# Performance work log

Measured on AMD Instinct MI355X. Metric: run time of the kernel, lower is better.

The kernel has to match this reference:

```python
import jax, jax.numpy as jnp
import numpy as np

BATCH = 2048
K = 64          # num_clusters
D = 128         # latent_dim / cluster_dim
R1 = 1024
OUT_LEN = 512   # output_length
IN_LEN = 512    # input_length
MIN_CLAMP = 0.0


def setup_inputs() -> dict:
    key = jax.random.key(0)
    k1, k2, k3, k4, k5, k6 = jax.random.split(key, 6)
    z = jax.random.normal(k1, (BATCH, 1, D), dtype=jnp.float32)
    u = jax.random.normal(k2, (BATCH, 1, R1), dtype=jnp.float32)
    member = jax.random.uniform(k3, (BATCH, 1, K), dtype=jnp.float32)
    # parameters
    mu = jax.random.uniform(k4, (K, D), dtype=jnp.float32)  # 1 * torch.rand
    sigma_inv = 10.0 * jnp.broadcast_to(jnp.eye(D, dtype=jnp.float32), (K, D, D))  # zeros with diag 10
    # nn.Linear default init: U(-1/sqrt(fan_in), 1/sqrt(fan_in)), weight shape (out, in)
    bound = 1.0 / np.sqrt(R1)
    W_con = jax.random.uniform(k5, (K, OUT_LEN, R1), dtype=jnp.float32, minval=-bound, maxval=bound)
    W_recon = jax.random.uniform(k6, (K, IN_LEN, R1), dtype=jnp.float32, minval=-bound, maxval=bound)
    return {"z": z, "u": u, "member": member, "mu": mu, "sigma_inv": sigma_inv,
            "W_con": W_con, "W_recon": W_recon}


def _compute_psi(z, mu, sigma_inv):
    # z: (B,1,D), mu: (K,D) -> d: (B,K,D)
    d = mu[None, :, :] - z
    # S = sigma_inv @ sigma_inv^T per cluster: (K,D,D)
    S = jnp.einsum('kde,kfe->kdf', sigma_inv, sigma_inv)
    # Mahalanobis: d^T S d per (b,k)
    d2 = jnp.einsum('bkd,kde,bke->bk', d, S, d)
    d2 = jnp.maximum(d2, MIN_CLAMP)
    psi = jax.nn.softmax(-d2, axis=1)  # (B,K)
    return psi


def reference(z, u, member, mu, sigma_inv, W_con, W_recon):
    psi = _compute_psi(z, mu, sigma_inv)          # (B,K)
    u2 = u[:, 0, :]                                # (B,R1)
    # grouped GEMM + abs: per-cluster |Linear(u)|
    y_LLM = jnp.abs(jnp.einsum('bi,koi->bko', u2, W_con))    # (B,K,OUT_LEN)
    x_LLM = jnp.abs(jnp.einsum('bi,koi->bko', u2, W_recon))  # (B,K,IN_LEN)
    mem = member[:, 0, :]                          # (B,K)
    y_con = jnp.einsum('bk,bko->bo', psi, y_LLM)[:, None, :]   # (B,1,OUT_LEN)
    x_recon = jnp.einsum('bk,bko->bo', mem, x_LLM)[:, None, :]  # (B,1,IN_LEN)
    return (y_con, x_recon)
```

## Files before the change

### kernel.cpp

```cpp
#include <hip/hip_runtime.h>
#include <hip/hip_bf16.h>
#include <stdint.h>

typedef __bf16 bf16_t;
typedef __bf16 bf16x8 __attribute__((ext_vector_type(8)));
typedef __bf16 bf16x4 __attribute__((ext_vector_type(4)));
typedef float  v4f    __attribute__((ext_vector_type(4)));
typedef float  f32x4  __attribute__((ext_vector_type(4)));

#define GLDS16(gp, lp)                                                         \
  __builtin_amdgcn_global_load_lds(                                            \
      (__attribute__((address_space(1))) void*)(gp),                           \
      (__attribute__((address_space(3))) void*)(lp), 16, 0, 0)

#define BATCH 2048
#define KEXP  64
#define NOUT  512
#define R1    1024

__global__ __launch_bounds__(256) void cast_u_k(const float* __restrict__ u,
                                                bf16_t* __restrict__ ub) {
  int idx = blockIdx.x * 256 + threadIdx.x;
  float4 v = ((const float4*)u)[idx];
  bf16x4 o;
  o.x = (bf16_t)v.x; o.y = (bf16_t)v.y; o.z = (bf16_t)v.z; o.w = (bf16_t)v.w;
  ((bf16x4*)ub)[idx] = o;
}

__global__ __launch_bounds__(256) void cast_w_k(const float* __restrict__ wcon,
                                                const float* __restrict__ wrec,
                                                bf16_t* __restrict__ wb) {
  const size_t tid = (size_t)blockIdx.x * 256 + threadIdx.x;
#pragma unroll
  for (int it = 0; it < 8; ++it) {
    size_t idx = tid + (size_t)it * (8192u * 256u);
    size_t e = idx << 2;
    int k = (int)(e >> 20);
    int n = (int)((e >> 10) & 1023);
    int i = (int)(e & 1023);
    const float* src = (n < NOUT)
        ? (wcon + (((size_t)k * NOUT + n) << 10) + i)
        : (wrec + (((size_t)k * NOUT + (n - NOUT)) << 10) + i);
    f32x4 v = __builtin_nontemporal_load((const f32x4*)src);
    bf16x4 o;
    o.x = (bf16_t)v.x; o.y = (bf16_t)v.y; o.z = (bf16_t)v.z; o.w = (bf16_t)v.w;
    ((bf16x4*)wb)[idx] = o;
  }
}

__global__ __launch_bounds__(256) void psi_d2_k(const float* __restrict__ z,
                                                const float* __restrict__ mu,
                                                const float* __restrict__ sig,
                                                float* __restrict__ d2g) {
  __shared__ float dv[64][132];
  __shared__ float Ss[16][128];
  const int t = threadIdx.x;
  const int k = blockIdx.x;
  const int b0 = blockIdx.y * 64;

  const float* muk = mu + k * 128;
#pragma unroll
  for (int i = 0; i < 8; ++i) {
    int f4 = i * 256 + t;
    int row = f4 >> 5, c4 = f4 & 31;
    float4 zq = ((const float4*)(z + (size_t)(b0 + row) * 128))[c4];
    float4 mq = ((const float4*)muk)[c4];
    float4 dq;
    dq.x = mq.x - zq.x; dq.y = mq.y - zq.y;
    dq.z = mq.z - zq.z; dq.w = mq.w - zq.w;
    *(float4*)&dv[row][c4 * 4] = dq;
  }

  const int et = t & 15, bt = t >> 4;
  const float* Sk = sig + ((size_t)k << 14);
  float acc[4][8];
#pragma unroll
  for (int j = 0; j < 4; ++j)
#pragma unroll
    for (int i = 0; i < 8; ++i) acc[j][i] = 0.f;

  for (int dblk = 0; dblk < 8; ++dblk) {
    __syncthreads();
#pragma unroll
    for (int i = 0; i < 2; ++i) {
      int f4 = i * 256 + t;
      int row = f4 >> 5, c4 = f4 & 31;
      *(float4*)&Ss[row][c4 * 4] =
          ((const float4*)(Sk + (size_t)(dblk * 16 + row) * 128))[c4];
    }
    __syncthreads();

#pragma unroll
    for (int d4 = 0; d4 < 4; ++d4) {
      float4 a[4];
#pragma unroll
      for (int j = 0; j < 4; ++j)
        a[j] = *(const float4*)&dv[bt * 4 + j][dblk * 16 + d4 * 4];
#pragma unroll
      for (int dd = 0; dd < 4; ++dd) {
        float4 s0 = *(const float4*)&Ss[d4 * 4 + dd][et * 8];
        float4 s1 = *(const float4*)&Ss[d4 * 4 + dd][et * 8 + 4];
        float av[4] = {a[0][dd], a[1][dd], a[2][dd], a[3][dd]};
#pragma unroll
        for (int j = 0; j < 4; ++j) {
          acc[j][0] = fmaf(s0.x, av[j], acc[j][0]);
          acc[j][1] = fmaf(s0.y, av[j], acc[j][1]);
          acc[j][2] = fmaf(s0.z, av[j], acc[j][2]);
          acc[j][3] = fmaf(s0.w, av[j], acc[j][3]);
          acc[j][4] = fmaf(s1.x, av[j], acc[j][4]);
          acc[j][5] = fmaf(s1.y, av[j], acc[j][5]);
          acc[j][6] = fmaf(s1.z, av[j], acc[j][6]);
          acc[j][7] = fmaf(s1.w, av[j], acc[j][7]);
        }
      }
    }
  }

  float v2[4];
#pragma unroll
  for (int j = 0; j < 4; ++j) {
    float s = 0.f;
#pragma unroll
    for (int i = 0; i < 8; ++i) s = fmaf(acc[j][i], acc[j][i], s);
    v2[j] = s;
  }
#pragma unroll
  for (int j = 0; j < 4; ++j) {
    v2[j] += __shfl_xor(v2[j], 1);
    v2[j] += __shfl_xor(v2[j], 2);
    v2[j] += __shfl_xor(v2[j], 4);
    v2[j] += __shfl_xor(v2[j], 8);
  }
  if (et == 0) {
#pragma unroll
    for (int j = 0; j < 4; ++j)
      d2g[(size_t)(b0 + bt * 4 + j) * 64 + k] = v2[j];
  }
}

__global__ __launch_bounds__(256) void psi_sm_k(const float* __restrict__ d2g,
                                                float* __restrict__ psi) {
  const int b = blockIdx.x * 4 + (threadIdx.x >> 6);
  const int lane = threadIdx.x & 63;
  float x = fmaxf(d2g[(size_t)b * 64 + lane], 0.0f);
  float m = x;
  m = fminf(m, __shfl_xor(m, 1));  m = fminf(m, __shfl_xor(m, 2));
  m = fminf(m, __shfl_xor(m, 4));  m = fminf(m, __shfl_xor(m, 8));
  m = fminf(m, __shfl_xor(m, 16)); m = fminf(m, __shfl_xor(m, 32));
  float ex = __expf(m - x);
  float s = ex;
  s += __shfl_xor(s, 1);  s += __shfl_xor(s, 2);  s += __shfl_xor(s, 4);
  s += __shfl_xor(s, 8);  s += __shfl_xor(s, 16); s += __shfl_xor(s, 32);
  psi[(size_t)b * 64 + lane] = ex / s;
}

__global__ __launch_bounds__(256, 2)
void fused_gemm(const bf16_t* __restrict__ ub,
                const bf16_t* __restrict__ wb,
                const float* __restrict__ psi,
                const float* __restrict__ member,
                float* __restrict__ out) {
  __shared__ bf16_t Alds[128 * 64];
  __shared__ bf16_t Blds[128 * 64];
  __shared__ float wlds[128];

  const int t = threadIdx.x, lane = t & 63, wv = t >> 6;
  const int bm0 = blockIdx.x * 128;
  const int n0  = blockIdx.y * 128;
  const int e0  = blockIdx.z * 8;
  const bool is_y = (n0 < NOUT);
  const float* wsel = is_y ? psi : member;
  const int wm = wv & 1, wn = wv >> 1;
  const int l15 = lane & 15, quad = lane >> 4;

  v4f acc[4][4], oacc[4][4];
#pragma unroll
  for (int mi = 0; mi < 4; ++mi)
#pragma unroll
    for (int ni = 0; ni < 4; ++ni)
#pragma unroll
      for (int r = 0; r < 4; ++r) { acc[mi][ni][r] = 0.f; oacc[mi][ni][r] = 0.f; }

  const int rA = wv * 8 + (lane >> 3);
  const int c8 = (((lane & 7) ^ (lane >> 3)) * 8);
  const bf16_t* au  = ub + (size_t)(bm0 + rA) * R1 + c8;
  const bf16_t* bw0 = wb + (size_t)(n0 + rA) * R1 + c8;

  const int fsw = l15 & 7;

  for (int ke = 0; ke < 8; ++ke) {
    const int ex = e0 + ke;
    const bf16_t* bw = bw0 + ((size_t)ex << 20);
    for (int kk = 0; kk < R1; kk += 64) {
      __syncthreads();
      if (kk == 0 && t < 128) wlds[t] = wsel[(size_t)(bm0 + t) * 64 + ex];
#pragma unroll
      for (int j = 0; j < 4; ++j) {
        GLDS16(au + (size_t)(j * 32) * R1 + kk, &Alds[(j * 32 + wv * 8) * 64]);
        GLDS16(bw + (size_t)(j * 32) * R1 + kk, &Blds[(j * 32 + wv * 8) * 64]);
      }
      __syncthreads();

      const bf16_t* Ab = &Alds[(wm * 64 + l15) * 64];
      const bf16_t* Bb = &Blds[(wn * 64 + l15) * 64];
#pragma unroll
      for (int ks = 0; ks < 2; ++ks) {
        const int co = ((ks * 4 + quad) ^ fsw) * 8;
        bf16x8 af[4], bfr[4];
#pragma unroll
        for (int i = 0; i < 4; ++i) {
          af[i]  = *(const bf16x8*)(Ab + i * 16 * 64 + co);
          bfr[i] = *(const bf16x8*)(Bb + i * 16 * 64 + co);
        }
#pragma unroll
        for (int mi = 0; mi < 4; ++mi)
#pragma unroll
          for (int ni = 0; ni < 4; ++ni)
            acc[mi][ni] = __builtin_amdgcn_mfma_f32_16x16x32_bf16(
                af[mi], bfr[ni], acc[mi][ni], 0, 0, 0);
      }
    }
#pragma unroll
    for (int mi = 0; mi < 4; ++mi) {
      float wr[4];
#pragma unroll
      for (int r = 0; r < 4; ++r) wr[r] = wlds[wm * 64 + mi * 16 + quad * 4 + r];
#pragma unroll
      for (int ni = 0; ni < 4; ++ni)
#pragma unroll
        for (int r = 0; r < 4; ++r) {
          oacc[mi][ni][r] += fabsf(acc[mi][ni][r]) * wr[r];
          acc[mi][ni][r] = 0.f;
        }
    }
  }

  float* obase = is_y ? out : out + (size_t)BATCH * NOUT;
  const int oc = (is_y ? n0 : n0 - NOUT) + wn * 64 + l15;
#pragma unroll
  for (int mi = 0; mi < 4; ++mi)
#pragma unroll
    for (int ni = 0; ni < 4; ++ni)
#pragma unroll
      for (int r = 0; r < 4; ++r) {
        int brow = bm0 + wm * 64 + mi * 16 + quad * 4 + r;
        atomicAdd(&obase[(size_t)brow * NOUT + oc + ni * 16], oacc[mi][ni][r]);
      }
}

extern "C" void kernel_launch(void* const* d_in, const int* in_sizes, int n_in,
                              void* d_out, int out_size, void* d_ws, size_t ws_size,
                              hipStream_t stream) {
  const float* z    = (const float*)d_in[0];
  const float* u    = (const float*)d_in[1];
  const float* mem  = (const float*)d_in[2];
  const float* mu   = (const float*)d_in[3];
  const float* sig  = (const float*)d_in[4];
  const float* wcon = (const float*)d_in[5];
  const float* wrec = (const float*)d_in[6];
  float* out = (float*)d_out;

  char* ws = (char*)d_ws;
  bf16_t* ub  = (bf16_t*)ws;
  bf16_t* wb  = (bf16_t*)(ws + ((size_t)4 << 20));
  float*  psw = (float*)(ws + ((size_t)132 << 20));
  float*  d2g = (float*)(ws + ((size_t)132 << 20) + ((size_t)512 << 10));

  hipMemsetAsync(d_out, 0, (size_t)out_size * sizeof(float), stream);
  cast_u_k<<<2048, 256, 0, stream>>>(u, ub);
  cast_w_k<<<8192, 256, 0, stream>>>(wcon, wrec, wb);
  psi_d2_k<<<dim3(64, 32), 256, 0, stream>>>(z, mu, sig, d2g);
  psi_sm_k<<<512, 256, 0, stream>>>(d2g, psw);
  fused_gemm<<<dim3(16, 8, 8), 256, 0, stream>>>(ub, wb, psw, mem, out);
}
```

Measured before the change: 677.8 us.

## Double-buffer LDS tiles with async prefetch and halve the expert-split grid

Moves the fused grouped GEMM from a single LDS buffer with two barriers per k-step to a two-stage software pipeline. Global-to-LDS loads for step s+2 are issued between the two MFMA halves, and explicit waitcnt, sched_barrier and setprio control the ordering. Each block now handles 16 experts instead of 8, which halves the grid and the number of output atomics, and all per-expert weights are loaded into LDS once at the start. This doubles LDS use and leaves fewer blocks, which may lower occupancy or CU coverage, and the hand-written waitcnt accounting is easy to get wrong.

```diff
diff --git a/kernel.cpp b/kernel.cpp
--- a/kernel.cpp
+++ b/kernel.cpp
@@ -160,18 +160,19 @@
                 const float* __restrict__ psi,
                 const float* __restrict__ member,
                 float* __restrict__ out) {
-  __shared__ bf16_t Alds[128 * 64];
-  __shared__ bf16_t Blds[128 * 64];
-  __shared__ float wlds[128];
+  __shared__ bf16_t Alds[2][128 * 64];
+  __shared__ bf16_t Blds[2][128 * 64];
+  __shared__ float  wlds[16][128];
 
   const int t = threadIdx.x, lane = t & 63, wv = t >> 6;
   const int bm0 = blockIdx.x * 128;
   const int n0  = blockIdx.y * 128;
-  const int e0  = blockIdx.z * 8;
+  const int e0  = blockIdx.z * 16;
   const bool is_y = (n0 < NOUT);
   const float* wsel = is_y ? psi : member;
   const int wm = wv & 1, wn = wv >> 1;
   const int l15 = lane & 15, quad = lane >> 4;
+  const int fsw = l15 & 7;
 
   v4f acc[4][4], oacc[4][4];
 #pragma unroll
@@ -186,45 +187,96 @@
   const bf16_t* au  = ub + (size_t)(bm0 + rA) * R1 + c8;
   const bf16_t* bw0 = wb + (size_t)(n0 + rA) * R1 + c8;
 
-  const int fsw = l15 & 7;
-
-  for (int ke = 0; ke < 8; ++ke) {
-    const int ex = e0 + ke;
-    const bf16_t* bw = bw0 + ((size_t)ex << 20);
-    for (int kk = 0; kk < R1; kk += 64) {
-      __syncthreads();
-      if (kk == 0 && t < 128) wlds[t] = wsel[(size_t)(bm0 + t) * 64 + ex];
-#pragma unroll
-      for (int j = 0; j < 4; ++j) {
-        GLDS16(au + (size_t)(j * 32) * R1 + kk, &Alds[(j * 32 + wv * 8) * 64]);
-        GLDS16(bw + (size_t)(j * 32) * R1 + kk, &Blds[(j * 32 + wv * 8) * 64]);
+  const int aoff = (wm * 64 + l15) * 64;
+  const int boff = (wn * 64 + l15) * 64;
+  const int co0 = (quad ^ fsw) * 8;
+  const int co1 = ((4 + quad) ^ fsw) * 8;
+
+  auto STAGE = [&](int s2, int p) {
+    const int ex2 = e0 + (s2 >> 4);
+    const int kk2 = (s2 & 15) << 6;
+    const bf16_t* a = au + kk2;
+    const bf16_t* b = bw0 + ((size_t)ex2 << 20) + kk2;
+    bf16_t* Ad = &Alds[p][wv * 8 * 64];
+    bf16_t* Bd = &Blds[p][wv * 8 * 64];
+#pragma unroll
+    for (int j = 0; j < 4; ++j)
+      GLDS16(a + (size_t)(j * 32) * R1, Ad + j * 32 * 64);
+#pragma unroll
+    for (int j = 0; j < 4; ++j)
+      GLDS16(b + (size_t)(j * 32) * R1, Bd + j * 32 * 64);
+  };
+
+  {
+    const int r = t >> 1, h = (t & 1) * 8;
+    const float* src = wsel + (size_t)(bm0 + r) * 64 + e0 + h;
+    f32x4 v0 = *(const f32x4*)src;
+    f32x4 v1 = *(const f32x4*)(src + 4);
+#pragma unroll
+    for (int j = 0; j < 4; ++j) { wlds[h + j][r] = v0[j]; wlds[h + 4 + j][r] = v1[j]; }
+  }
+  STAGE(0, 0);
+  STAGE(1, 1);
+  asm volatile("s_waitcnt vmcnt(8) lgkmcnt(0)" ::: "memory");
+  __builtin_amdgcn_s_barrier();
+
+  for (int ke = 0; ke < 16; ++ke) {
+#pragma unroll 2
+    for (int kt = 0; kt < 16; ++kt) {
+      const int p = kt & 1;
+      const int s = (ke << 4) + kt;
+      const bf16_t* Ap = &Alds[p][aoff];
+      const bf16_t* Bp = &Blds[p][boff];
+
+      bf16x8 a0[4], b0[4];
+#pragma unroll
+      for (int i = 0; i < 4; ++i) {
+        a0[i] = *(const bf16x8*)(Ap + i * 16 * 64 + co0);
+        b0[i] = *(const bf16x8*)(Bp + i * 16 * 64 + co0);
       }
-      __syncthreads();
-
-      const bf16_t* Ab = &Alds[(wm * 64 + l15) * 64];
-      const bf16_t* Bb = &Blds[(wn * 64 + l15) * 64];
-#pragma unroll
-      for (int ks = 0; ks < 2; ++ks) {
-        const int co = ((ks * 4 + quad) ^ fsw) * 8;
-        bf16x8 af[4], bfr[4];
-#pragma unroll
-        for (int i = 0; i < 4; ++i) {
-          af[i]  = *(const bf16x8*)(Ab + i * 16 * 64 + co);
-          bfr[i] = *(const bf16x8*)(Bb + i * 16 * 64 + co);
-        }
-#pragma unroll
-        for (int mi = 0; mi < 4; ++mi)
-#pragma unroll
-          for (int ni = 0; ni < 4; ++ni)
-            acc[mi][ni] = __builtin_amdgcn_mfma_f32_16x16x32_bf16(
-                af[mi], bfr[ni], acc[mi][ni], 0, 0, 0);
+      asm volatile("s_waitcnt lgkmcnt(0)" ::: "memory");
+      __builtin_amdgcn_sched_barrier(0);
+      __builtin_amdgcn_s_setprio(1);
+#pragma unroll
+      for (int mi = 0; mi < 4; ++mi)
+#pragma unroll
+        for (int ni = 0; ni < 4; ++ni)
+          acc[mi][ni] = __builtin_amdgcn_mfma_f32_16x16x32_bf16(
+              a0[mi], b0[ni], acc[mi][ni], 0, 0, 0);
+      __builtin_amdgcn_s_setprio(0);
+
+      bf16x8 a1[4], b1[4];
+#pragma unroll
+      for (int i = 0; i < 4; ++i) {
+        a1[i] = *(const bf16x8*)(Ap + i * 16 * 64 + co1);
+        b1[i] = *(const bf16x8*)(Bp + i * 16 * 64 + co1);
       }
+      asm volatile("s_waitcnt lgkmcnt(0)" ::: "memory");
+      __builtin_amdgcn_sched_barrier(0);
+      __builtin_amdgcn_s_barrier();
+
+      int s2 = s + 2; s2 = (s2 > 255) ? 255 : s2;
+      STAGE(s2, p);
+
+      __builtin_amdgcn_s_setprio(1);
+#pragma unroll
+      for (int mi = 0; mi < 4; ++mi)
+#pragma unroll
+        for (int ni = 0; ni < 4; ++ni)
+          acc[mi][ni] = __builtin_amdgcn_mfma_f32_16x16x32_bf16(
+              a1[mi], b1[ni], acc[mi][ni], 0, 0, 0);
+      __builtin_amdgcn_s_setprio(0);
+
+      asm volatile("s_waitcnt vmcnt(8)" ::: "memory");
+      __builtin_amdgcn_s_barrier();
     }
+
 #pragma unroll
     for (int mi = 0; mi < 4; ++mi) {
       float wr[4];
 #pragma unroll
-      for (int r = 0; r < 4; ++r) wr[r] = wlds[wm * 64 + mi * 16 + quad * 4 + r];
+      for (int r = 0; r < 4; ++r)
+        wr[r] = wlds[ke][wm * 64 + mi * 16 + quad * 4 + r];
 #pragma unroll
       for (int ni = 0; ni < 4; ++ni)
 #pragma unroll
@@ -246,6 +298,7 @@
         int brow = bm0 + wm * 64 + mi * 16 + quad * 4 + r;
         atomicAdd(&obase[(size_t)brow * NOUT + oc + ni * 16], oacc[mi][ni][r]);
       }
+  asm volatile("s_waitcnt vmcnt(0)" ::: "memory");
 }
 
 extern "C" void kernel_launch(void* const* d_in, const int* in_sizes, int n_in,
@@ -271,5 +324,5 @@
   cast_w_k<<<8192, 256, 0, stream>>>(wcon, wrec, wb);
   psi_d2_k<<<dim3(64, 32), 256, 0, stream>>>(z, mu, sig, d2g);
   psi_sm_k<<<512, 256, 0, stream>>>(d2g, psw);
-  fused_gemm<<<dim3(16, 8, 8), 256, 0, stream>>>(ub, wb, psw, mem, out);
-}
+  fused_gemm<<<dim3(16, 8, 4), 256, 0, stream>>>(ub, wb, psw, mem, out);
+}
```

Measured after the change: 634.1 us. 1.07x faster.
